# Kernel tuning notes

Hardware: AMD Instinct MI355X
Metric: run time of the kernel (lower is better)

Reference implementation:

```python
import jax, jax.numpy as jnp
import numpy as np

D_MODEL = 1024
N_HEADS = 16
D_K = D_MODEL // N_HEADS
BATCH = 2
SEQ = 2048


def setup_inputs() -> dict:
    key = jax.random.key(0)
    ks = jax.random.split(key, 9)
    s = 1.0 / np.sqrt(D_MODEL)
    x = jax.random.normal(ks[0], (BATCH, SEQ, D_MODEL), dtype=jnp.float32)
    # nn.Linear params: weight [out, in], bias [out]
    w_q = jax.random.uniform(ks[1], (D_MODEL, D_MODEL), jnp.float32, -s, s)
    b_q = jax.random.uniform(ks[2], (D_MODEL,), jnp.float32, -s, s)
    w_k = jax.random.uniform(ks[3], (D_MODEL, D_MODEL), jnp.float32, -s, s)
    b_k = jax.random.uniform(ks[4], (D_MODEL,), jnp.float32, -s, s)
    w_v = jax.random.uniform(ks[5], (D_MODEL, D_MODEL), jnp.float32, -s, s)
    b_v = jax.random.uniform(ks[6], (D_MODEL,), jnp.float32, -s, s)
    w_o = jax.random.uniform(ks[7], (D_MODEL, D_MODEL), jnp.float32, -s, s)
    b_o = jax.random.uniform(ks[8], (D_MODEL,), jnp.float32, -s, s)
    return {"x": x, "w_q": w_q, "b_q": b_q, "w_k": w_k, "b_k": b_k,
            "w_v": w_v, "b_v": b_v, "w_o": w_o, "b_o": b_o}


def reference(x, w_q, b_q, w_k, b_k, w_v, b_v, w_o, b_o):
    B, S, _ = x.shape
    # Linear projections, then split heads: [B, H, S, d_k]
    def proj(w, b):
        y = jnp.einsum('bsd,ed->bse', x, w) + b
        return y.reshape(B, S, N_HEADS, D_K).transpose(0, 2, 1, 3)
    q = proj(w_q, b_q)
    k = proj(w_k, b_k)
    v = proj(w_v, b_v)
    scores = jnp.einsum('bhqd,bhkd->bhqk', q, k) / jnp.sqrt(jnp.float32(D_K))
    attn = jax.nn.softmax(scores, axis=-1)  # dropout is identity in eval mode
    out = jnp.einsum('bhqk,bhkd->bhqd', attn, v)
    out = out.transpose(0, 2, 1, 3).reshape(B, S, D_MODEL)
    out = jnp.einsum('bsd,ed->bse', out, w_o) + b_o
    return out, attn
```

## Files before the change

### kernel.cpp

```cpp
#include <hip/hip_runtime.h>
#include <hip/hip_bf16.h>
#include <stdint.h>


typedef __attribute__((ext_vector_type(4))) float f32x4;
typedef __attribute__((ext_vector_type(8))) short s16x8;
typedef __attribute__((ext_vector_type(4))) unsigned short u16x4;

#define MFMA(a, b, c) __builtin_amdgcn_mfma_f32_16x16x32_bf16((a), (b), (c), 0, 0, 0)

__device__ __forceinline__ unsigned short f2bf(float f) {
    unsigned int u = __float_as_uint(f);
    unsigned int r = (u + 0x7FFFu + ((u >> 16) & 1u)) >> 16;
    return (unsigned short)r;
}

__global__ void convert_kernel(const float* __restrict__ x,
                               const float* __restrict__ wq, const float* __restrict__ wk,
                               const float* __restrict__ wv, const float* __restrict__ wo,
                               unsigned short* __restrict__ xb, unsigned short* __restrict__ wb) {
    size_t g = (size_t)blockIdx.x * blockDim.x + threadIdx.x;
    size_t i4 = g * 4;
    const float* src;
    unsigned short* dst;
    size_t off;
    if (i4 < 4194304) {
        src = x; dst = xb; off = i4;
    } else {
        size_t j = i4 - 4194304;
        int wsel = (int)(j >> 20);
        off = j & 1048575;
        src = (wsel == 0) ? wq : (wsel == 1) ? wk : (wsel == 2) ? wv : wo;
        dst = wb + ((size_t)wsel << 20);
    }
    float4 v = *(const float4*)(src + off);
    u16x4 o;
    o[0] = f2bf(v.x); o[1] = f2bf(v.y); o[2] = f2bf(v.z); o[3] = f2bf(v.w);
    *(u16x4*)(dst + off) = o;
}

__global__ __launch_bounds__(256, 3) void gemm_kernel(
    const unsigned short* __restrict__ A, const unsigned short* __restrict__ B,
    const float* __restrict__ bias_q, const float* __restrict__ bias_k,
    const float* __restrict__ bias_v, int mode,
    unsigned short* __restrict__ Qs, unsigned short* __restrict__ Kb,
    unsigned short* __restrict__ Vt, float* __restrict__ outp) {
    const int t = threadIdx.x;
    const int lane = t & 63;
    const int wv4 = t >> 6;
    const int wr = wv4 >> 1, wc = wv4 & 1;
    const int rowbase = blockIdx.y * 128;
    const int colbase = blockIdx.x * 128;

    __shared__ __align__(16) unsigned short lA[128 * 64];
    __shared__ __align__(16) unsigned short lB[128 * 64];

    const int crow = lane >> 3;
    const int ccol = (lane & 7) * 8;

    f32x4 acc[4][4];
#pragma unroll
    for (int mi = 0; mi < 4; ++mi)
#pragma unroll
        for (int ni = 0; ni < 4; ++ni)
            acc[mi][ni] = (f32x4){0.f, 0.f, 0.f, 0.f};

    const int l15 = lane & 15;
    const int koff = (lane >> 4) * 8;
    const int ar = wr * 64 + l15;
    const int br = wc * 64 + l15;

    for (int kt = 0; kt < 16; ++kt) {
        const int kbase = kt * 64 + ccol;
#pragma unroll
        for (int i = 0; i < 4; ++i) {
            const int c = wv4 * 4 + i;
            const int r = c * 8 + crow;
            __builtin_amdgcn_global_load_lds(
                (const __attribute__((address_space(1))) void*)(A + (size_t)(rowbase + r) * 1024 + kbase),
                (__attribute__((address_space(3))) void*)&lA[c * 512], 16, 0, 0);
            __builtin_amdgcn_global_load_lds(
                (const __attribute__((address_space(1))) void*)(B + (size_t)(colbase + r) * 1024 + kbase),
                (__attribute__((address_space(3))) void*)&lB[c * 512], 16, 0, 0);
        }
        __syncthreads();
#pragma unroll
        for (int kk = 0; kk < 2; ++kk) {
            s16x8 af[4], bf[4];
#pragma unroll
            for (int mi = 0; mi < 4; ++mi)
                af[mi] = *(const s16x8*)&lA[(ar + mi * 16) * 64 + kk * 32 + koff];
#pragma unroll
            for (int ni = 0; ni < 4; ++ni)
                bf[ni] = *(const s16x8*)&lB[(br + ni * 16) * 64 + kk * 32 + koff];
#pragma unroll
            for (int mi = 0; mi < 4; ++mi)
#pragma unroll
                for (int ni = 0; ni < 4; ++ni)
                    acc[mi][ni] = MFMA(af[mi], bf[ni], acc[mi][ni]);
        }
        __syncthreads();
    }

    if (mode == 1) {
#pragma unroll
        for (int ni = 0; ni < 4; ++ni) {
            int n = colbase + wc * 64 + ni * 16 + l15;
            float bv = bias_q[n];
#pragma unroll
            for (int mi = 0; mi < 4; ++mi) {
#pragma unroll
                for (int reg = 0; reg < 4; ++reg) {
                    int m = rowbase + wr * 64 + mi * 16 + (lane >> 4) * 4 + reg;
                    outp[(size_t)m * 1024 + n] = acc[mi][ni][reg] + bv;
                }
            }
        }
    } else {
        const int proj = colbase >> 10;
        const float* bias = (proj == 0) ? bias_q : (proj == 1) ? bias_k : bias_v;
        const float scale = (proj == 0) ? 0.18033688011112042f : 1.0f;
#pragma unroll
        for (int ni = 0; ni < 4; ++ni) {
            int n = colbase + wc * 64 + ni * 16 + l15;
            int nn = n & 1023;
            int h = nn >> 6, d = nn & 63;
            float bv = bias[nn];
#pragma unroll
            for (int mi = 0; mi < 4; ++mi) {
                int m0 = rowbase + wr * 64 + mi * 16 + (lane >> 4) * 4;
                int b = m0 >> 11, s0 = m0 & 2047;
                if (proj == 2) {
                    u16x4 pk;
#pragma unroll
                    for (int reg = 0; reg < 4; ++reg)
                        pk[reg] = f2bf(acc[mi][ni][reg] + bv);
                    *(u16x4*)&Vt[((size_t)(b * 16 + h) * 64 + d) * 2048 + s0] = pk;
                } else {
                    unsigned short* dstp = (proj == 0) ? Qs : Kb;
#pragma unroll
                    for (int reg = 0; reg < 4; ++reg)
                        dstp[((size_t)(b * 16 + h) * 2048 + (s0 + reg)) * 64 + d] =
                            f2bf((acc[mi][ni][reg] + bv) * scale);
                }
            }
        }
    }
}

__global__ __launch_bounds__(256, 2) void attn_kernel(
    const unsigned short* __restrict__ Qs, const unsigned short* __restrict__ Kb,
    const unsigned short* __restrict__ Vt, float* __restrict__ attn,
    unsigned short* __restrict__ ctx) {
    const int t = threadIdx.x;
    const int lane = t & 63;
    const int l15 = lane & 15;
    const int g = lane >> 4;
    const int g4 = g * 4, g8 = g * 8;
    const int w = t >> 6;
    const int wr = w >> 1, wc = w & 1;
    const int qt = blockIdx.x;
    const int bh = blockIdx.y;
    const int b = bh >> 4, h = bh & 15;

    const unsigned short* Qh = Qs + (size_t)bh * (2048 * 64);
    const unsigned short* Kh = Kb + (size_t)bh * (2048 * 64);
    const unsigned short* Vh = Vt + (size_t)bh * (64 * 2048);
    float* attn_h = attn + (size_t)bh * (2048 * 2048) + (size_t)(qt * 128) * 2048;

    __shared__ unsigned short lP[2][128 * 72];
    __shared__ float lred[2][128];

    s16x8 qf[8];
#pragma unroll
    for (int mi = 0; mi < 4; ++mi)
#pragma unroll
        for (int kk = 0; kk < 2; ++kk)
            qf[mi * 2 + kk] =
                *(const s16x8*)&Qh[(size_t)(qt * 128 + wr * 64 + mi * 16 + l15) * 64 + kk * 32 + g8];

    s16x8 kf0[4], kf1[4], vf0[4], vf1[4];

#define K_LOAD(DST, KT)                                                                     \
    {                                                                                       \
        _Pragma("unroll") for (int ni = 0; ni < 2; ++ni)                                    \
            _Pragma("unroll") for (int kk = 0; kk < 2; ++kk)                                \
                DST[ni * 2 + kk] = *(const s16x8*)&Kh[(size_t)((KT) * 64 + wc * 32 +        \
                                                               ni * 16 + l15) * 64 +        \
                                                      kk * 32 + g8];                        \
    }
#define V_LOAD(DST, KT)                                                                     \
    {                                                                                       \
        _Pragma("unroll") for (int ni = 0; ni < 2; ++ni)                                    \
            _Pragma("unroll") for (int ks = 0; ks < 2; ++ks)                                \
                DST[ni * 2 + ks] = *(const s16x8*)&Vh[(size_t)(wc * 32 + ni * 16 + l15) *   \
                                                          2048 +                            \
                                                      (KT) * 64 + ks * 32 + g8];            \
    }
#define QK_MFMA(KF, SACC)                                                                   \
    {                                                                                       \
        _Pragma("unroll") for (int kk = 0; kk < 2; ++kk)                                    \
            _Pragma("unroll") for (int mi = 0; mi < 4; ++mi)                                \
                _Pragma("unroll") for (int ni = 0; ni < 2; ++ni)                            \
                    SACC[mi][ni] = MFMA(KF[ni * 2 + kk], qf[mi * 2 + kk], SACC[mi][ni]);    \
    }

    float qsum[4] = {0.f, 0.f, 0.f, 0.f};
    K_LOAD(kf0, 0);
#define P1_BODY(KF, KFN, KT)                                                                \
    {                                                                                       \
        f32x4 sacc[4][2];                                                                   \
        _Pragma("unroll") for (int mi = 0; mi < 4; ++mi)                                    \
            _Pragma("unroll") for (int ni = 0; ni < 2; ++ni)                                \
                sacc[mi][ni] = (f32x4){0.f, 0.f, 0.f, 0.f};                                 \
        QK_MFMA(KF, sacc);                                                                  \
        if ((KT) < 31) K_LOAD(KFN, (KT) + 1);                                               \
        _Pragma("unroll") for (int mi = 0; mi < 4; ++mi) {                                  \
            float e = 0.f;                                                                  \
            _Pragma("unroll") for (int ni = 0; ni < 2; ++ni)                                \
                _Pragma("unroll") for (int r = 0; r < 4; ++r)                               \
                    e += exp2f(sacc[mi][ni][r]);                                            \
            qsum[mi] += e;                                                                  \
        }                                                                                   \
    }
    for (int k2 = 0; k2 < 16; ++k2) {
        P1_BODY(kf0, kf1, 2 * k2);
        P1_BODY(kf1, kf0, 2 * k2 + 1);
    }
#pragma unroll
    for (int mi = 0; mi < 4; ++mi) {
        float v = qsum[mi];
        v += __shfl_xor(v, 16);
        v += __shfl_xor(v, 32);
        qsum[mi] = v;
    }
    if (lane < 16) {
#pragma unroll
        for (int mi = 0; mi < 4; ++mi)
            lred[wc][wr * 64 + mi * 16 + lane] = qsum[mi];
    }
    __syncthreads();
    float rl[4];
#pragma unroll
    for (int mi = 0; mi < 4; ++mi) {
        int q = wr * 64 + mi * 16 + l15;
        rl[mi] = 1.0f / (lred[0][q] + lred[1][q]);
    }

    f32x4 oacc[4][2];
#pragma unroll
    for (int mi = 0; mi < 4; ++mi)
#pragma unroll
        for (int ni = 0; ni < 2; ++ni) oacc[mi][ni] = (f32x4){0.f, 0.f, 0.f, 0.f};

    K_LOAD(kf0, 0);
    V_LOAD(vf0, 0);
#define P2_BODY(BUF, KF, KFN, VF, VFN, KT)                                                  \
    {                                                                                       \
        f32x4 sacc[4][2];                                                                   \
        _Pragma("unroll") for (int mi = 0; mi < 4; ++mi)                                    \
            _Pragma("unroll") for (int ni = 0; ni < 2; ++ni)                                \
                sacc[mi][ni] = (f32x4){0.f, 0.f, 0.f, 0.f};                                 \
        QK_MFMA(KF, sacc);                                                                  \
        if ((KT) < 31) {                                                                    \
            K_LOAD(KFN, (KT) + 1);                                                          \
            V_LOAD(VFN, (KT) + 1);                                                          \
        }                                                                                   \
        _Pragma("unroll") for (int mi = 0; mi < 4; ++mi) {                                  \
            const int q = wr * 64 + mi * 16 + l15;                                          \
            _Pragma("unroll") for (int ni = 0; ni < 2; ++ni) {                              \
                float4 pv;                                                                  \
                pv.x = exp2f(sacc[mi][ni][0]) * rl[mi];                                     \
                pv.y = exp2f(sacc[mi][ni][1]) * rl[mi];                                     \
                pv.z = exp2f(sacc[mi][ni][2]) * rl[mi];                                     \
                pv.w = exp2f(sacc[mi][ni][3]) * rl[mi];                                     \
                *(float4*)&attn_h[(size_t)q * 2048 + (KT) * 64 + wc * 32 + ni * 16 + g4] =  \
                    pv;                                                                     \
                u16x4 pk;                                                                   \
                pk[0] = f2bf(pv.x);                                                         \
                pk[1] = f2bf(pv.y);                                                         \
                pk[2] = f2bf(pv.z);                                                         \
                pk[3] = f2bf(pv.w);                                                         \
                *(u16x4*)&lP[BUF][q * 72 + wc * 32 + ni * 16 + g4] = pk;                    \
            }                                                                               \
        }                                                                                   \
        __syncthreads();                                                                    \
        _Pragma("unroll") for (int ks = 0; ks < 2; ++ks) {                                  \
            s16x8 pf[4];                                                                    \
            _Pragma("unroll") for (int mi = 0; mi < 4; ++mi)                                \
                pf[mi] =                                                                    \
                    *(const s16x8*)&lP[BUF][(wr * 64 + mi * 16 + l15) * 72 + ks * 32 + g8]; \
            _Pragma("unroll") for (int mi = 0; mi < 4; ++mi)                                \
                _Pragma("unroll") for (int ni = 0; ni < 2; ++ni)                            \
                    oacc[mi][ni] = MFMA(pf[mi], VF[ni * 2 + ks], oacc[mi][ni]);             \
        }                                                                                   \
    }
    for (int k2 = 0; k2 < 16; ++k2) {
        P2_BODY(0, kf0, kf1, vf0, vf1, 2 * k2);
        P2_BODY(1, kf1, kf0, vf1, vf0, 2 * k2 + 1);
    }

#pragma unroll
    for (int mi = 0; mi < 4; ++mi) {
#pragma unroll
        for (int ni = 0; ni < 2; ++ni) {
            int d = wc * 32 + ni * 16 + l15;
#pragma unroll
            for (int r = 0; r < 4; ++r) {
                int q = qt * 128 + wr * 64 + mi * 16 + g4 + r;
                ctx[((size_t)(b * 2048 + q)) * 1024 + h * 64 + d] = f2bf(oacc[mi][ni][r]);
            }
        }
    }
#undef K_LOAD
#undef V_LOAD
#undef QK_MFMA
#undef P1_BODY
#undef P2_BODY
}

extern "C" void kernel_launch(void* const* d_in, const int* in_sizes, int n_in,
                              void* d_out, int out_size, void* d_ws, size_t ws_size,
                              hipStream_t stream) {
    const float* x  = (const float*)d_in[0];
    const float* wq = (const float*)d_in[1];
    const float* bq = (const float*)d_in[2];
    const float* wk = (const float*)d_in[3];
    const float* bk = (const float*)d_in[4];
    const float* wv = (const float*)d_in[5];
    const float* bv = (const float*)d_in[6];
    const float* wo = (const float*)d_in[7];
    const float* bo = (const float*)d_in[8];

    char* ws = (char*)d_ws;
    unsigned short* xb  = (unsigned short*)(ws);
    unsigned short* wb  = (unsigned short*)(ws + 8388608);
    unsigned short* Qsc = (unsigned short*)(ws + 16777216);
    unsigned short* Kb  = (unsigned short*)(ws + 25165824);
    unsigned short* Vt  = (unsigned short*)(ws + 33554432);
    unsigned short* ctx = (unsigned short*)(ws + 41943040);

    float* out  = (float*)d_out;
    float* attn = out + 4194304;

    convert_kernel<<<8192, 256, 0, stream>>>(x, wq, wk, wv, wo, xb, wb);
    gemm_kernel<<<dim3(24, 32), 256, 0, stream>>>(xb, wb, bq, bk, bv, 0,
                                                  Qsc, Kb, Vt, nullptr);
    attn_kernel<<<dim3(16, 32), 256, 0, stream>>>(Qsc, Kb, Vt, attn, ctx);
    gemm_kernel<<<dim3(8, 32), 256, 0, stream>>>(ctx, wb + 3 * 1048576, bo, bo, bo, 1,
                                                 nullptr, nullptr, nullptr, out);
}
```

Measured before the change: 279.2 us.

## Keep P in registers for PV MFMA via permuted V layout and split-K reduction

```diff
diff --git a/kernel.cpp b/kernel.cpp
--- a/kernel.cpp
+++ b/kernel.cpp
@@ -5,6 +5,7 @@
 
 typedef __attribute__((ext_vector_type(4))) float f32x4;
 typedef __attribute__((ext_vector_type(8))) short s16x8;
+typedef __attribute__((ext_vector_type(8))) unsigned short u16x8;
 typedef __attribute__((ext_vector_type(4))) unsigned short u16x4;
 
 #define MFMA(a, b, c) __builtin_amdgcn_mfma_f32_16x16x32_bf16((a), (b), (c), 0, 0, 0)
@@ -135,7 +136,10 @@
 #pragma unroll
                     for (int reg = 0; reg < 4; ++reg)
                         pk[reg] = f2bf(acc[mi][ni][reg] + bv);
-                    *(u16x4*)&Vt[((size_t)(b * 16 + h) * 64 + d) * 2048 + s0] = pk;
+                    int j0 = s0 & 31;
+                    int pg = (j0 >> 2) & 3, pn = (j0 >> 4) & 1;
+                    int pcol = (s0 & ~31) | (pg << 3) | (pn << 2);
+                    *(u16x4*)&Vt[((size_t)(b * 16 + h) * 64 + d) * 2048 + pcol] = pk;
                 } else {
                     unsigned short* dstp = (proj == 0) ? Qs : Kb;
 #pragma unroll
@@ -168,8 +172,8 @@
     const unsigned short* Vh = Vt + (size_t)bh * (64 * 2048);
     float* attn_h = attn + (size_t)bh * (2048 * 2048) + (size_t)(qt * 128) * 2048;
 
-    __shared__ unsigned short lP[2][128 * 72];
     __shared__ float lred[2][128];
+    __shared__ float lO[2][64 * 65];
 
     s16x8 qf[8];
 #pragma unroll
@@ -191,11 +195,9 @@
     }
 #define V_LOAD(DST, KT)                                                                     \
     {                                                                                       \
-        _Pragma("unroll") for (int ni = 0; ni < 2; ++ni)                                    \
-            _Pragma("unroll") for (int ks = 0; ks < 2; ++ks)                                \
-                DST[ni * 2 + ks] = *(const s16x8*)&Vh[(size_t)(wc * 32 + ni * 16 + l15) *   \
-                                                          2048 +                            \
-                                                      (KT) * 64 + ks * 32 + g8];            \
+        _Pragma("unroll") for (int db = 0; db < 4; ++db)                                    \
+            DST[db] = *(const s16x8*)&Vh[(size_t)(db * 16 + l15) * 2048 +                   \
+                                         (KT) * 64 + wc * 32 + g8];                         \
     }
 #define QK_MFMA(KF, SACC)                                                                   \
     {                                                                                       \
@@ -247,15 +249,15 @@
         rl[mi] = 1.0f / (lred[0][q] + lred[1][q]);
     }
 
-    f32x4 oacc[4][2];
+    f32x4 oacc[4][4];
 #pragma unroll
     for (int mi = 0; mi < 4; ++mi)
 #pragma unroll
-        for (int ni = 0; ni < 2; ++ni) oacc[mi][ni] = (f32x4){0.f, 0.f, 0.f, 0.f};
+        for (int db = 0; db < 4; ++db) oacc[mi][db] = (f32x4){0.f, 0.f, 0.f, 0.f};
 
     K_LOAD(kf0, 0);
     V_LOAD(vf0, 0);
-#define P2_BODY(BUF, KF, KFN, VF, VFN, KT)                                                  \
+#define P2_BODY(KF, KFN, VF, VFN, KT)                                                       \
     {                                                                                       \
         f32x4 sacc[4][2];                                                                   \
         _Pragma("unroll") for (int mi = 0; mi < 4; ++mi)                                    \
@@ -266,8 +268,10 @@
             K_LOAD(KFN, (KT) + 1);                                                          \
             V_LOAD(VFN, (KT) + 1);                                                          \
         }                                                                                   \
+        s16x8 pf[4];                                                                        \
         _Pragma("unroll") for (int mi = 0; mi < 4; ++mi) {                                  \
             const int q = wr * 64 + mi * 16 + l15;                                          \
+            u16x8 pk;                                                                       \
             _Pragma("unroll") for (int ni = 0; ni < 2; ++ni) {                              \
                 float4 pv;                                                                  \
                 pv.x = exp2f(sacc[mi][ni][0]) * rl[mi];                                     \
@@ -276,39 +280,43 @@
                 pv.w = exp2f(sacc[mi][ni][3]) * rl[mi];                                     \
                 *(float4*)&attn_h[(size_t)q * 2048 + (KT) * 64 + wc * 32 + ni * 16 + g4] =  \
                     pv;                                                                     \
-                u16x4 pk;                                                                   \
-                pk[0] = f2bf(pv.x);                                                         \
-                pk[1] = f2bf(pv.y);                                                         \
-                pk[2] = f2bf(pv.z);                                                         \
-                pk[3] = f2bf(pv.w);                                                         \
-                *(u16x4*)&lP[BUF][q * 72 + wc * 32 + ni * 16 + g4] = pk;                    \
+                pk[ni * 4 + 0] = f2bf(pv.x);                                                \
+                pk[ni * 4 + 1] = f2bf(pv.y);                                                \
+                pk[ni * 4 + 2] = f2bf(pv.z);                                                \
+                pk[ni * 4 + 3] = f2bf(pv.w);                                                \
             }                                                                               \
+            pf[mi] = *(const s16x8*)&pk;                                                    \
         }                                                                                   \
-        __syncthreads();                                                                    \
-        _Pragma("unroll") for (int ks = 0; ks < 2; ++ks) {                                  \
-            s16x8 pf[4];                                                                    \
-            _Pragma("unroll") for (int mi = 0; mi < 4; ++mi)                                \
-                pf[mi] =                                                                    \
-                    *(const s16x8*)&lP[BUF][(wr * 64 + mi * 16 + l15) * 72 + ks * 32 + g8]; \
-            _Pragma("unroll") for (int mi = 0; mi < 4; ++mi)                                \
-                _Pragma("unroll") for (int ni = 0; ni < 2; ++ni)                            \
-                    oacc[mi][ni] = MFMA(pf[mi], VF[ni * 2 + ks], oacc[mi][ni]);             \
-        }                                                                                   \
+        _Pragma("unroll") for (int mi = 0; mi < 4; ++mi)                                    \
+            _Pragma("unroll") for (int db = 0; db < 4; ++db)                                \
+                oacc[mi][db] = MFMA(pf[mi], VF[db], oacc[mi][db]);                          \
     }
     for (int k2 = 0; k2 < 16; ++k2) {
-        P2_BODY(0, kf0, kf1, vf0, vf1, 2 * k2);
-        P2_BODY(1, kf1, kf0, vf1, vf0, 2 * k2 + 1);
-    }
-
-#pragma unroll
-    for (int mi = 0; mi < 4; ++mi) {
-#pragma unroll
-        for (int ni = 0; ni < 2; ++ni) {
-            int d = wc * 32 + ni * 16 + l15;
-#pragma unroll
-            for (int r = 0; r < 4; ++r) {
-                int q = qt * 128 + wr * 64 + mi * 16 + g4 + r;
-                ctx[((size_t)(b * 2048 + q)) * 1024 + h * 64 + d] = f2bf(oacc[mi][ni][r]);
+        P2_BODY(kf0, kf1, vf0, vf1, 2 * k2);
+        P2_BODY(kf1, kf0, vf1, vf0, 2 * k2 + 1);
+    }
+
+    if (wc == 1) {
+#pragma unroll
+        for (int mi = 0; mi < 4; ++mi)
+#pragma unroll
+            for (int db = 0; db < 4; ++db)
+#pragma unroll
+                for (int r = 0; r < 4; ++r)
+                    lO[wr][(mi * 16 + g4 + r) * 65 + db * 16 + l15] = oacc[mi][db][r];
+    }
+    __syncthreads();
+    if (wc == 0) {
+#pragma unroll
+        for (int mi = 0; mi < 4; ++mi) {
+#pragma unroll
+            for (int db = 0; db < 4; ++db) {
+#pragma unroll
+                for (int r = 0; r < 4; ++r) {
+                    float s = oacc[mi][db][r] + lO[wr][(mi * 16 + g4 + r) * 65 + db * 16 + l15];
+                    int q = qt * 128 + wr * 64 + mi * 16 + g4 + r;
+                    ctx[((size_t)(b * 2048 + q)) * 1024 + h * 64 + db * 16 + l15] = f2bf(s);
+                }
             }
         }
     }
```

New measurement: 283.3 us. Within noise of the previous version (+1.4%).
